# Kernel tuning notes

Hardware: AMD Instinct MI355X
Metric: run time of the kernel (lower is better)

## Reference

```python
import jax, jax.numpy as jnp
import numpy as np

IMAGE_SIZE = 1920
NMS_PRE = 3000
NMS_POST = 300
THRESHOLD = 0.5
RATIOS = (0.5, 1.0, 2.0)
SCALES = (8.0, 16.0, 32.0)


def _generate_anchors(stride, H, W):
    # Standard RPN-style grid anchors: [H, W, K, 4] in (x1, y1, x2, y2).
    ratios = jnp.asarray(RATIOS, jnp.float32)
    scales = jnp.asarray(SCALES, jnp.float32)
    ws = (stride * scales[None, :] / jnp.sqrt(ratios)[:, None]).reshape(-1)  # [K]
    hs = (stride * scales[None, :] * jnp.sqrt(ratios)[:, None]).reshape(-1)  # [K]
    cx = (jnp.arange(W, dtype=jnp.float32) + 0.5) * stride
    cy = (jnp.arange(H, dtype=jnp.float32) + 0.5) * stride
    cyg, cxg = jnp.meshgrid(cy, cx, indexing="ij")  # [H, W]
    x1 = cxg[..., None] - 0.5 * ws
    y1 = cyg[..., None] - 0.5 * hs
    x2 = cxg[..., None] + 0.5 * ws
    y2 = cyg[..., None] + 0.5 * hs
    return jnp.stack([x1, y1, x2, y2], axis=-1)  # [H, W, K, 4]


def _nms_keep(boxes, scores):
    # Greedy NMS on score-sorted boxes [P,4]; returns bool keep mask [P].
    boxes = jax.lax.stop_gradient(boxes)
    P = boxes.shape[0]
    x1, y1, x2, y2 = boxes[:, 0], boxes[:, 1], boxes[:, 2], boxes[:, 3]
    areas = (x2 - x1 + 1.0) * (y2 - y1 + 1.0)
    xx1 = jnp.maximum(x1[:, None], x1[None, :])
    yy1 = jnp.maximum(y1[:, None], y1[None, :])
    xx2 = jnp.minimum(x2[:, None], x2[None, :])
    yy2 = jnp.minimum(y2[:, None], y2[None, :])
    inter = jnp.maximum(xx2 - xx1 + 1.0, 0.0) * jnp.maximum(yy2 - yy1 + 1.0, 0.0)
    iou = inter / (areas[:, None] + areas[None, :] - inter)  # [P, P]
    idx = jnp.arange(P)

    def body(keep, i):
        sup = (iou[i] > THRESHOLD) & (idx > i) & keep[i]
        return keep & ~sup, None

    keep, _ = jax.lax.scan(body, jnp.ones((P,), bool), jnp.arange(P))
    return keep


def _select(keep, boxes, scores):
    # First NMS_POST kept entries, zero padded (matches pad_tensor).
    rank = jnp.cumsum(keep) - 1
    valid = keep & (rank < NMS_POST)
    pos = jnp.where(valid, rank, NMS_POST)  # invalid -> scratch slot
    b = jnp.zeros((NMS_POST + 1, 4), boxes.dtype).at[pos].set(
        jnp.where(valid[:, None], boxes, 0.0))[:NMS_POST]
    s = jnp.zeros((NMS_POST + 1,), scores.dtype).at[pos].set(
        jnp.where(valid, scores, 0.0))[:NMS_POST]
    return b, s


def _forward(cls_scores, bbox_deltas):
    N, K, H, W = cls_scores.shape
    stride = float(int(round(IMAGE_SIZE / float(W))))
    anchors = _generate_anchors(stride, H, W)  # [H, W, K, 4]
    # [N, 4K, H, W] -> [N, H, W, K, 4]; decode is a plain add, as in the source.
    deltas = bbox_deltas.transpose(0, 2, 3, 1).reshape(N, H, W, K, 4)
    regions = anchors[None] + deltas  # [N, H, W, K, 4]
    # permute(0,2,3,1) then permute(0,3,1,2) is the identity on cls_scores.
    scores = cls_scores.reshape(N, -1)  # [N, K*H*W]
    # Faithful replication of the torch .view memory reinterpretation:
    # contiguous [N,H,W,K,4] viewed as [N,K,4,H,W], permuted, flattened.
    regions = regions.reshape(N, K, 4, H, W).transpose(0, 3, 4, 1, 2).reshape(N, -1, 4)
    # cross_boundary(..., remove=False): clip boxes to the image.
    regions = jnp.clip(regions, 0.0, IMAGE_SIZE - 1.0)
    pre = min(NMS_PRE, scores.shape[1])
    top_scores, order = jax.lax.top_k(scores, pre)  # sorted desc, like torch.topk
    regions_top = jnp.take_along_axis(regions, order[:, :, None], axis=1)  # [N, pre, 4]
    keep = jax.vmap(_nms_keep)(regions_top, top_scores)  # [N, pre] bool
    boxes_out, scores_out = jax.vmap(_select)(keep, regions_top, top_scores)
    # Faithful to the source bug: `output[:, :, 0] = ...` inside the batch loop
    # overwrites the score column for ALL images each iteration, so the final
    # score column equals the last image's padded scores, broadcast over N.
    score_col = jnp.broadcast_to(scores_out[-1][None, :, None], (N, NMS_POST, 1))
    return jnp.concatenate([score_col, boxes_out], axis=-1)  # [N, NMS_POST, 5]


def setup_inputs() -> dict:
    key = jax.random.key(0)
    k1, k2 = jax.random.split(key)
    cls_scores = jax.random.normal(k1, (8, 9, 120, 120), dtype=jnp.float32)
    bbox_deltas = jax.random.normal(k2, (8, 36, 120, 120), dtype=jnp.float32) * 8.0
    return {"cls_scores": cls_scores, "bbox_deltas": bbox_deltas}


def reference(cls_scores, bbox_deltas):
    return _forward(cls_scores, bbox_deltas)
```

## Files before the change

### kernel.cpp

```cpp
#include <hip/hip_runtime.h>
#include <stdint.h>

#define A_TOTAL 129600
#define NBATCH 8
#define PRE 3000
#define POST 300
#define NWORD 47
#define CAP 6144
#define NTILE 1128
#define HBLK 32
#define JCHUNK 768

typedef unsigned long long u64;

__device__ __forceinline__ unsigned xform(float f) {
    unsigned b = __float_as_uint(f);
    return (b & 0x80000000u) ? ~b : (b | 0x80000000u);
}
__device__ __forceinline__ float unxform(unsigned u) {
    return __uint_as_float((u & 0x80000000u) ? (u & 0x7FFFFFFFu) : ~u);
}
__device__ __forceinline__ u64 readlane64(u64 v, int l) {
    unsigned lo = (unsigned)__builtin_amdgcn_readlane((int)(unsigned)v, l);
    unsigned hi = (unsigned)__builtin_amdgcn_readlane((int)(unsigned)(v >> 32), l);
    return ((u64)hi << 32) | lo;
}

__global__ void zero_kernel(unsigned* __restrict__ ghist, int* __restrict__ ccount,
                            int* __restrict__ grank) {
    int g = blockIdx.x * blockDim.x + threadIdx.x;
    if (g < NBATCH * 4096) ghist[g] = 0u;
    else if (g < NBATCH * 4096 + NBATCH) ccount[g - NBATCH * 4096] = 0;
    else if (g < NBATCH * 4096 + NBATCH + NBATCH * CAP)
        grank[g - NBATCH * 4096 - NBATCH] = 0;
}

__global__ __launch_bounds__(256) void hist1_kernel(const float* __restrict__ cls,
                                                    unsigned* __restrict__ ghist) {
    const int n = blockIdx.y;
    __shared__ unsigned h[4096];
    for (int i = threadIdx.x; i < 4096; i += 256) h[i] = 0u;
    __syncthreads();
    const float4* c4 = (const float4*)(cls + (size_t)n * A_TOTAL);
    const int n4 = A_TOTAL / 4;
    for (int i = blockIdx.x * 256 + threadIdx.x; i < n4; i += HBLK * 256) {
        float4 v = c4[i];
        atomicAdd(&h[xform(v.x) >> 20], 1u);
        atomicAdd(&h[xform(v.y) >> 20], 1u);
        atomicAdd(&h[xform(v.z) >> 20], 1u);
        atomicAdd(&h[xform(v.w) >> 20], 1u);
    }
    __syncthreads();
    unsigned* gh = ghist + n * 4096;
    for (int i = threadIdx.x; i < 4096; i += 256)
        if (h[i]) atomicAdd(&gh[i], h[i]);
}

__global__ __launch_bounds__(256) void pick1_kernel(const unsigned* __restrict__ ghist,
                                                    unsigned* __restrict__ state) {
    const int n = blockIdx.x;
    const int tid = threadIdx.x;
    __shared__ unsigned gsum[256];
    const unsigned* gh = ghist + n * 4096;
    unsigned s = 0;
    for (int q = 0; q < 16; ++q) s += gh[tid * 16 + q];
    gsum[tid] = s;
    __syncthreads();
    if (tid == 0) {
        unsigned acc = 0; int g = 255;
        for (; g > 0; --g) { if (acc + gsum[g] >= PRE) break; acc += gsum[g]; }
        int b = 16 * g + 15;
        for (; b >= 16 * g; --b) { if (acc + gh[b] >= PRE) break; acc += gh[b]; }
        state[n] = ((unsigned)b) << 20;
    }
}

__global__ __launch_bounds__(256) void compact_kernel(const float* __restrict__ cls,
                                                      const unsigned* __restrict__ state,
                                                      u64* __restrict__ cand,
                                                      int* __restrict__ ccount) {
    const int n = blockIdx.y;
    const int tid = threadIdx.x;
    __shared__ u64 lbuf[4096];
    __shared__ unsigned lcnt, lbase;
    if (tid == 0) lcnt = 0u;
    __syncthreads();
    const unsigned uT = state[n];
    const float4* c4 = (const float4*)(cls + (size_t)n * A_TOTAL);
    const int n4 = A_TOTAL / 4;
    for (int i = blockIdx.x * 256 + tid; i < n4; i += HBLK * 256) {
        float4 v = c4[i];
        const float* vf = (const float*)&v;
#pragma unroll
        for (int c = 0; c < 4; ++c) {
            unsigned u = xform(vf[c]);
            if (u >= uT) {
                unsigned slot = atomicAdd(&lcnt, 1u);
                if (slot < 4096u)
                    lbuf[slot] = ((u64)u << 32) | (unsigned)(~(4 * i + c));
            }
        }
    }
    __syncthreads();
    if (tid == 0) lbase = (unsigned)atomicAdd(&ccount[n], (int)min(lcnt, 4096u));
    __syncthreads();
    const unsigned cnt = min(lcnt, 4096u), base = lbase;
    u64* cd = cand + (size_t)n * CAP;
    for (unsigned j = tid; j < cnt; j += 256)
        if (base + j < CAP) cd[base + j] = lbuf[j];
}

__global__ __launch_bounds__(256) void ranksort_partial(const u64* __restrict__ cand,
                                                        const int* __restrict__ ccount,
                                                        int* __restrict__ grank) {
    const int n = blockIdx.z;
    const int C = min(ccount[n], CAP);
    if (blockIdx.x * 256 >= C) return;
    const int j0 = blockIdx.y * JCHUNK;
    if (j0 >= C) return;
    const int tid = threadIdx.x;
    __shared__ u64 k[JCHUNK];
    const u64* cd = cand + (size_t)n * CAP;
    const int jlim = min(JCHUNK, C - j0);
    for (int j = tid; j < JCHUNK; j += 256)
        k[j] = (j < jlim) ? cd[j0 + j] : 0ull;
    __syncthreads();
    const int i = blockIdx.x * 256 + tid;
    if (i >= C) return;
    const u64 key = cd[i];
    int rank = 0;
    int j = 0;
    for (; j + 8 <= JCHUNK; j += 8) {
        rank += (k[j] > key) + (k[j+1] > key) + (k[j+2] > key) + (k[j+3] > key)
              + (k[j+4] > key) + (k[j+5] > key) + (k[j+6] > key) + (k[j+7] > key);
    }
    if (rank) atomicAdd(&grank[n * CAP + i], rank);
}

__global__ __launch_bounds__(256) void rank_gather(const u64* __restrict__ cand,
                                                   const int* __restrict__ ccount,
                                                   const int* __restrict__ grank,
                                                   const float* __restrict__ bbox,
                                                   float* __restrict__ tscores,
                                                   float* __restrict__ boxes) {
    const int n = blockIdx.y;
    const int C = min(ccount[n], CAP);
    const int i = blockIdx.x * 256 + threadIdx.x;
    if (i >= C) return;
    const int rank = grank[n * CAP + i];
    if (rank >= PRE) return;
    const u64 key = cand[(size_t)n * CAP + i];
    const unsigned u = (unsigned)(key >> 32);
    const int r = (int)(~(unsigned)key);
    tscores[n * PRE + rank] = unxform(u);

    int kp = r % 9;
    int pp = r / 9;
    int s_ch = pp % 36;
    int qbase = pp / 36;
    int k2 = s_ch >> 2, j2 = s_ch & 3;
    float ratio = (k2 < 3) ? 0.5f : ((k2 < 6) ? 1.0f : 2.0f);
    int si = k2 % 3;
    float scale = (si == 0) ? 8.0f : ((si == 1) ? 16.0f : 32.0f);
    float sq = sqrtf(ratio);
    float wsk = 16.0f * scale / sq;
    float hsk = 16.0f * scale * sq;
    float* outp = boxes + ((size_t)n * PRE + rank) * 4;
#pragma unroll
    for (int j4 = 0; j4 < 4; ++j4) {
        int c = 4 * kp + j4;
        int q = c * 400 + qbase;
        int hh = q / 120, w2 = q % 120;
        float cx = (w2 + 0.5f) * 16.0f;
        float cy = (hh + 0.5f) * 16.0f;
        float a;
        if (j2 == 0)      a = cx - 0.5f * wsk;
        else if (j2 == 1) a = cy - 0.5f * hsk;
        else if (j2 == 2) a = cx + 0.5f * wsk;
        else              a = cy + 0.5f * hsk;
        float d = bbox[((size_t)n * 36 + s_ch) * 14400 + q];
        outp[j4] = fminf(fmaxf(a + d, 0.0f), 1919.0f);
    }
}

__global__ __launch_bounds__(256) void nms_mask_kernel(const float* __restrict__ boxes,
                                                       u64* __restrict__ mask) {
    const int n = blockIdx.y;
    const int t = threadIdx.x & 63;
    const int wv = threadIdx.x >> 6;
    const int T = blockIdx.x * 4 + wv;
    const bool active = (T < NTILE);
    __shared__ float cx1[4][64], cy1[4][64], cx2[4][64], cy2[4][64], car[4][64];
    int rb = 0, cb = 0;
    if (active) {
        int off = 0;
        for (int r = 0; r < NWORD; ++r) {
            int row_tiles = NWORD - r;
            if (T < off + row_tiles) { rb = r; cb = r + (T - off); break; }
            off += row_tiles;
        }
        int cj = cb * 64 + t;
        if (cj < PRE) {
            float4 b4 = *(const float4*)(boxes + ((size_t)n * PRE + cj) * 4);
            cx1[wv][t] = b4.x; cy1[wv][t] = b4.y; cx2[wv][t] = b4.z; cy2[wv][t] = b4.w;
            car[wv][t] = (b4.z - b4.x + 1.0f) * (b4.w - b4.y + 1.0f);
        }
    }
    __syncthreads();
    if (!active) return;
    int i = rb * 64 + t;
    if (i >= PRE) return;
    float4 b4 = *(const float4*)(boxes + ((size_t)n * PRE + i) * 4);
    float x1 = b4.x, y1 = b4.y, x2 = b4.z, y2 = b4.w;
    float ai = (x2 - x1 + 1.0f) * (y2 - y1 + 1.0f);
    u64 w = 0ull;
    int lim = min(64, PRE - cb * 64);
    for (int jj = 0; jj < lim; ++jj) {
        float xx1 = fmaxf(x1, cx1[wv][jj]);
        float yy1 = fmaxf(y1, cy1[wv][jj]);
        float xx2 = fminf(x2, cx2[wv][jj]);
        float yy2 = fminf(y2, cy2[wv][jj]);
        float iw = fmaxf(xx2 - xx1 + 1.0f, 0.0f);
        float ih = fmaxf(yy2 - yy1 + 1.0f, 0.0f);
        float inter = iw * ih;
        float iou = inter / (ai + car[wv][jj] - inter);
        if (iou > 0.5f) w |= (1ull << jj);
    }
    mask[((size_t)n * PRE + i) * NWORD + cb] = w;
}

#define TSTRIDE 49
__global__ __launch_bounds__(256) void nms_scan_kernel(const u64* __restrict__ mask,
                                                       const float* __restrict__ tscores,
                                                       const float* __restrict__ boxes,
                                                       float* __restrict__ out) {
    const int n = blockIdx.x;
    const int tid = threadIdx.x;
    const int lane = tid & 63;
    const int wv = tid >> 6;
    __shared__ u64 tile[2][64 * TSTRIDE];
    __shared__ int kidx[POST];
    __shared__ int s_cnt;
    const u64* mrow = mask + (size_t)n * PRE * NWORD;

    for (int idx = tid; idx < 64 * NWORD; idx += 256) {
        int r = idx / NWORD, wd = idx % NWORD;
        tile[0][r * TSTRIDE + wd] = mrow[(size_t)r * NWORD + wd];
    }
    if (tid == 0) s_cnt = 0;
    __syncthreads();

    u64 rem = 0ull;
    for (int w = 0; w < NWORD; ++w) {
        const int buf = w & 1;
        if (wv > 0 && w + 1 < NWORD) {
            const int base = 64 * (w + 1);
            for (int idx = tid - 64; idx < 64 * NWORD; idx += 192) {
                int r = idx / NWORD, wd = idx % NWORD;
                int row = base + r;
                tile[buf ^ 1][r * TSTRIDE + wd] =
                    (row < PRE) ? mrow[(size_t)row * NWORD + wd] : 0ull;
            }
        }
        if (wv == 0) {
            int cnt = s_cnt;
            const int base = 64 * w;
            const int lim = min(64, PRE - base);
            u64 vrow = (lane < lim) ? tile[buf][lane * TSTRIDE + w] : 0ull;
            u64 cur = readlane64(rem, w);
            u64 todo = ~cur;
            if (lim < 64) todo &= (1ull << lim) - 1ull;
            u64 alive = 0ull;
            while (todo) {
                int b = __ffsll((long long)todo) - 1;
                if (lane == 0) kidx[cnt] = base + b;
                alive |= 1ull << b;
                cnt++;
                if (cnt >= POST) break;
                u64 sup = readlane64(vrow, b);
                todo &= ~(sup | (1ull << b));
            }
            if (lane < NWORD) {
                u64 t2 = alive;
                while (t2) {
                    int b0 = __ffsll((long long)t2) - 1; t2 &= t2 - 1;
                    int b1 = b0, b2 = b0, b3 = b0;
                    if (t2) { b1 = __ffsll((long long)t2) - 1; t2 &= t2 - 1; }
                    if (t2) { b2 = __ffsll((long long)t2) - 1; t2 &= t2 - 1; }
                    if (t2) { b3 = __ffsll((long long)t2) - 1; t2 &= t2 - 1; }
                    u64 a0 = tile[buf][b0 * TSTRIDE + lane];
                    u64 a1 = tile[buf][b1 * TSTRIDE + lane];
                    u64 a2 = tile[buf][b2 * TSTRIDE + lane];
                    u64 a3 = tile[buf][b3 * TSTRIDE + lane];
                    rem |= (a0 | a1) | (a2 | a3);
                }
            }
            if (lane == 0) s_cnt = cnt;
        }
        __syncthreads();
        if (s_cnt >= POST) break;
    }

    const int cnt = s_cnt;
    for (int t = tid; t < POST; t += 256) {
        float* op = out + ((size_t)n * POST + t) * 5;
        if (t < cnt) {
            int i = kidx[t];
            const float* bp = boxes + ((size_t)n * PRE + i) * 4;
            op[1] = bp[0]; op[2] = bp[1]; op[3] = bp[2]; op[4] = bp[3];
        } else {
            op[1] = 0.0f; op[2] = 0.0f; op[3] = 0.0f; op[4] = 0.0f;
        }
        if (n == NBATCH - 1) {
            float sv = (t < cnt) ? tscores[n * PRE + kidx[t]] : 0.0f;
            for (int m = 0; m < NBATCH; ++m)
                out[((size_t)m * POST + t) * 5] = sv;
        }
    }
}

extern "C" void kernel_launch(void* const* d_in, const int* in_sizes, int n_in,
                              void* d_out, int out_size, void* d_ws, size_t ws_size,
                              hipStream_t stream) {
    const float* cls = (const float*)d_in[0];
    const float* bbox = (const float*)d_in[1];
    float* out = (float*)d_out;

    char* p = (char*)d_ws;
    u64* mask = (u64*)p;
    unsigned* ghist = (unsigned*)p;
    unsigned* state = (unsigned*)(p + 131072);
    int* ccount = (int*)(p + 131200);
    u64* cand = (u64*)(p + 131584);
    int* grank = (int*)(p + 524800);
    float* tscores = (float*)(p + 9024000);
    float* boxes = (float*)(p + 9120000);
    (void)ws_size; (void)n_in; (void)in_sizes; (void)out_size;

    zero_kernel<<<(NBATCH * 4096 + NBATCH + NBATCH * CAP + 255) / 256, 256, 0, stream>>>(ghist, ccount, grank);
    hist1_kernel<<<dim3(HBLK, NBATCH), 256, 0, stream>>>(cls, ghist);
    pick1_kernel<<<NBATCH, 256, 0, stream>>>(ghist, state);
    compact_kernel<<<dim3(HBLK, NBATCH), 256, 0, stream>>>(cls, state, cand, ccount);
    ranksort_partial<<<dim3(CAP / 256, CAP / JCHUNK, NBATCH), 256, 0, stream>>>(cand, ccount, grank);
    rank_gather<<<dim3(CAP / 256, NBATCH), 256, 0, stream>>>(cand, ccount, grank, bbox, tscores, boxes);
    nms_mask_kernel<<<dim3((NTILE + 3) / 4, NBATCH), 256, 0, stream>>>(boxes, mask);
    nms_scan_kernel<<<NBATCH, 256, 0, stream>>>(mask, tscores, boxes, out);
}
```

Before: 182.3 us.

## Widen NMS scan windows to 192 rows and replace rank atomics with partial sums

The NMS scan now processes 192-row windows, three 64-bit words at a time, so the block runs 16 barrier-separated iterations instead of 47. The tile is stored unpadded and copied with float4 loads. The rank atomics are replaced by per-chunk partial rank arrays that rank_gather sums, which removes the zeroing kernel in favour of a memset plus resetting ccount in pick1. The trade-off is much larger LDS use (about 144 KB) and more register pressure in the serial scan loop.

```diff
diff --git a/kernel.cpp b/kernel.cpp
--- a/kernel.cpp
+++ b/kernel.cpp
@@ -10,6 +10,9 @@
 #define NTILE 1128
 #define HBLK 32
 #define JCHUNK 768
+#define NJC 8
+#define WW 192
+#define NWIN 16
 
 typedef unsigned long long u64;
 
@@ -24,15 +27,6 @@
     unsigned lo = (unsigned)__builtin_amdgcn_readlane((int)(unsigned)v, l);
     unsigned hi = (unsigned)__builtin_amdgcn_readlane((int)(unsigned)(v >> 32), l);
     return ((u64)hi << 32) | lo;
-}
-
-__global__ void zero_kernel(unsigned* __restrict__ ghist, int* __restrict__ ccount,
-                            int* __restrict__ grank) {
-    int g = blockIdx.x * blockDim.x + threadIdx.x;
-    if (g < NBATCH * 4096) ghist[g] = 0u;
-    else if (g < NBATCH * 4096 + NBATCH) ccount[g - NBATCH * 4096] = 0;
-    else if (g < NBATCH * 4096 + NBATCH + NBATCH * CAP)
-        grank[g - NBATCH * 4096 - NBATCH] = 0;
 }
 
 __global__ __launch_bounds__(256) void hist1_kernel(const float* __restrict__ cls,
@@ -57,7 +51,8 @@
 }
 
 __global__ __launch_bounds__(256) void pick1_kernel(const unsigned* __restrict__ ghist,
-                                                    unsigned* __restrict__ state) {
+                                                    unsigned* __restrict__ state,
+                                                    int* __restrict__ ccount) {
     const int n = blockIdx.x;
     const int tid = threadIdx.x;
     __shared__ unsigned gsum[256];
@@ -72,6 +67,7 @@
         int b = 16 * g + 15;
         for (; b >= 16 * g; --b) { if (acc + gh[b] >= PRE) break; acc += gh[b]; }
         state[n] = ((unsigned)b) << 20;
+        ccount[n] = 0;
     }
 }
 
@@ -112,7 +108,7 @@
 
 __global__ __launch_bounds__(256) void ranksort_partial(const u64* __restrict__ cand,
                                                         const int* __restrict__ ccount,
-                                                        int* __restrict__ grank) {
+                                                        int* __restrict__ grank_part) {
     const int n = blockIdx.z;
     const int C = min(ccount[n], CAP);
     if (blockIdx.x * 256 >= C) return;
@@ -134,12 +130,12 @@
         rank += (k[j] > key) + (k[j+1] > key) + (k[j+2] > key) + (k[j+3] > key)
               + (k[j+4] > key) + (k[j+5] > key) + (k[j+6] > key) + (k[j+7] > key);
     }
-    if (rank) atomicAdd(&grank[n * CAP + i], rank);
+    grank_part[((size_t)n * NJC + blockIdx.y) * CAP + i] = rank;
 }
 
 __global__ __launch_bounds__(256) void rank_gather(const u64* __restrict__ cand,
                                                    const int* __restrict__ ccount,
-                                                   const int* __restrict__ grank,
+                                                   const int* __restrict__ grank_part,
                                                    const float* __restrict__ bbox,
                                                    float* __restrict__ tscores,
                                                    float* __restrict__ boxes) {
@@ -147,7 +143,10 @@
     const int C = min(ccount[n], CAP);
     const int i = blockIdx.x * 256 + threadIdx.x;
     if (i >= C) return;
-    const int rank = grank[n * CAP + i];
+    const int nj = (C + JCHUNK - 1) / JCHUNK;
+    int rank = 0;
+    for (int jc = 0; jc < nj; ++jc)
+        rank += grank_part[((size_t)n * NJC + jc) * CAP + i];
     if (rank >= PRE) return;
     const u64 key = cand[(size_t)n * CAP + i];
     const unsigned u = (unsigned)(key >> 32);
@@ -229,7 +228,6 @@
     mask[((size_t)n * PRE + i) * NWORD + cb] = w;
 }
 
-#define TSTRIDE 49
 __global__ __launch_bounds__(256) void nms_scan_kernel(const u64* __restrict__ mask,
                                                        const float* __restrict__ tscores,
                                                        const float* __restrict__ boxes,
@@ -238,61 +236,89 @@
     const int tid = threadIdx.x;
     const int lane = tid & 63;
     const int wv = tid >> 6;
-    __shared__ u64 tile[2][64 * TSTRIDE];
+    __shared__ u64 tile[2][WW * NWORD];
     __shared__ int kidx[POST];
     __shared__ int s_cnt;
     const u64* mrow = mask + (size_t)n * PRE * NWORD;
 
-    for (int idx = tid; idx < 64 * NWORD; idx += 256) {
-        int r = idx / NWORD, wd = idx % NWORD;
-        tile[0][r * TSTRIDE + wd] = mrow[(size_t)r * NWORD + wd];
+    {
+        const float4* src = (const float4*)mrow;
+        float4* dst = (float4*)tile[0];
+        for (int i = tid; i < WW * NWORD / 2; i += 256) dst[i] = src[i];
     }
     if (tid == 0) s_cnt = 0;
     __syncthreads();
 
     u64 rem = 0ull;
-    for (int w = 0; w < NWORD; ++w) {
+    for (int w = 0; w < NWIN; ++w) {
         const int buf = w & 1;
-        if (wv > 0 && w + 1 < NWORD) {
-            const int base = 64 * (w + 1);
-            for (int idx = tid - 64; idx < 64 * NWORD; idx += 192) {
-                int r = idx / NWORD, wd = idx % NWORD;
-                int row = base + r;
-                tile[buf ^ 1][r * TSTRIDE + wd] =
-                    (row < PRE) ? mrow[(size_t)row * NWORD + wd] : 0ull;
-            }
+        const int base = WW * w;
+        if (wv > 0 && w + 1 < NWIN) {
+            const int nbase = base + WW;
+            const int nrows = min(WW, PRE - nbase);
+            const float4* src = (const float4*)(mrow + (size_t)nbase * NWORD);
+            float4* dst = (float4*)tile[buf ^ 1];
+            const int n4 = nrows * NWORD / 2;
+            for (int i = tid - 64; i < n4; i += 192) dst[i] = src[i];
         }
         if (wv == 0) {
             int cnt = s_cnt;
-            const int base = 64 * w;
-            const int lim = min(64, PRE - base);
-            u64 vrow = (lane < lim) ? tile[buf][lane * TSTRIDE + w] : 0ull;
-            u64 cur = readlane64(rem, w);
-            u64 todo = ~cur;
-            if (lim < 64) todo &= (1ull << lim) - 1ull;
-            u64 alive = 0ull;
-            while (todo) {
-                int b = __ffsll((long long)todo) - 1;
-                if (lane == 0) kidx[cnt] = base + b;
-                alive |= 1ull << b;
+            const int lim = min(WW, PRE - base);
+            const int w0 = 3 * w;
+            const bool q2ok = (w0 + 2 < NWORD);
+            u64 v00, v01, v02, v10, v11, v12, v20, v21, v22;
+            {
+                const u64* t0 = &tile[buf][(size_t)lane * NWORD + w0];
+                const u64* t1 = &tile[buf][(size_t)(lane + 64) * NWORD + w0];
+                const u64* t2 = &tile[buf][(size_t)(lane + 128) * NWORD + w0];
+                v00 = t0[0]; v01 = t0[1]; v02 = q2ok ? t0[2] : 0ull;
+                v10 = t1[0]; v11 = t1[1]; v12 = q2ok ? t1[2] : 0ull;
+                v20 = t2[0]; v21 = t2[1]; v22 = q2ok ? t2[2] : 0ull;
+            }
+            u64 todo0 = ~readlane64(rem, w0);
+            u64 todo1 = ~readlane64(rem, w0 + 1);
+            u64 todo2 = q2ok ? ~readlane64(rem, w0 + 2) : 0ull;
+            if (lim < 64)       { todo0 &= (1ull << lim) - 1; todo1 = 0; todo2 = 0; }
+            else if (lim < 128) { todo1 &= (1ull << (lim - 64)) - 1; todo2 = 0; }
+            else if (lim < 192) { todo2 &= (1ull << (lim - 128)) - 1; }
+            u64 alive0 = 0, alive1 = 0, alive2 = 0;
+            while (todo0 | todo1 | todo2) {
+                int q, b;
+                if (todo0)      { q = 0; b = __ffsll((long long)todo0) - 1; }
+                else if (todo1) { q = 1; b = __ffsll((long long)todo1) - 1; }
+                else            { q = 2; b = __ffsll((long long)todo2) - 1; }
+                const int p = q * 64 + b;
+                if (lane == 0) kidx[cnt] = base + p;
+                if (q == 0) alive0 |= 1ull << b;
+                else if (q == 1) alive1 |= 1ull << b;
+                else alive2 |= 1ull << b;
                 cnt++;
                 if (cnt >= POST) break;
-                u64 sup = readlane64(vrow, b);
-                todo &= ~(sup | (1ull << b));
+                u64 s0, s1, s2;
+                if (q == 0)      { s0 = readlane64(v00, b); s1 = readlane64(v01, b); s2 = readlane64(v02, b); }
+                else if (q == 1) { s0 = readlane64(v10, b); s1 = readlane64(v11, b); s2 = readlane64(v12, b); }
+                else             { s0 = readlane64(v20, b); s1 = readlane64(v21, b); s2 = readlane64(v22, b); }
+                todo0 &= ~s0; todo1 &= ~s1; todo2 &= ~s2;
+                if (q == 0) todo0 &= ~(1ull << b);
+                else if (q == 1) todo1 &= ~(1ull << b);
+                else todo2 &= ~(1ull << b);
             }
             if (lane < NWORD) {
-                u64 t2 = alive;
-                while (t2) {
-                    int b0 = __ffsll((long long)t2) - 1; t2 &= t2 - 1;
-                    int b1 = b0, b2 = b0, b3 = b0;
-                    if (t2) { b1 = __ffsll((long long)t2) - 1; t2 &= t2 - 1; }
-                    if (t2) { b2 = __ffsll((long long)t2) - 1; t2 &= t2 - 1; }
-                    if (t2) { b3 = __ffsll((long long)t2) - 1; t2 &= t2 - 1; }
-                    u64 a0 = tile[buf][b0 * TSTRIDE + lane];
-                    u64 a1 = tile[buf][b1 * TSTRIDE + lane];
-                    u64 a2 = tile[buf][b2 * TSTRIDE + lane];
-                    u64 a3 = tile[buf][b3 * TSTRIDE + lane];
-                    rem |= (a0 | a1) | (a2 | a3);
+                for (int q = 0; q < 3; ++q) {
+                    u64 t2m = (q == 0) ? alive0 : (q == 1) ? alive1 : alive2;
+                    const int roff = q * 64;
+                    while (t2m) {
+                        int b0 = __ffsll((long long)t2m) - 1; t2m &= t2m - 1;
+                        int b1 = b0, b2 = b0, b3 = b0;
+                        if (t2m) { b1 = __ffsll((long long)t2m) - 1; t2m &= t2m - 1; }
+                        if (t2m) { b2 = __ffsll((long long)t2m) - 1; t2m &= t2m - 1; }
+                        if (t2m) { b3 = __ffsll((long long)t2m) - 1; t2m &= t2m - 1; }
+                        u64 a0 = tile[buf][(size_t)(roff + b0) * NWORD + lane];
+                        u64 a1 = tile[buf][(size_t)(roff + b1) * NWORD + lane];
+                        u64 a2 = tile[buf][(size_t)(roff + b2) * NWORD + lane];
+                        u64 a3 = tile[buf][(size_t)(roff + b3) * NWORD + lane];
+                        rem |= (a0 | a1) | (a2 | a3);
+                    }
                 }
             }
             if (lane == 0) s_cnt = cnt;
@@ -332,17 +358,17 @@
     unsigned* state = (unsigned*)(p + 131072);
     int* ccount = (int*)(p + 131200);
     u64* cand = (u64*)(p + 131584);
-    int* grank = (int*)(p + 524800);
+    int* grank_part = (int*)(p + 524800);
     float* tscores = (float*)(p + 9024000);
     float* boxes = (float*)(p + 9120000);
     (void)ws_size; (void)n_in; (void)in_sizes; (void)out_size;
 
-    zero_kernel<<<(NBATCH * 4096 + NBATCH + NBATCH * CAP + 255) / 256, 256, 0, stream>>>(ghist, ccount, grank);
+    hipMemsetAsync(ghist, 0, 131072, stream);
     hist1_kernel<<<dim3(HBLK, NBATCH), 256, 0, stream>>>(cls, ghist);
-    pick1_kernel<<<NBATCH, 256, 0, stream>>>(ghist, state);
+    pick1_kernel<<<NBATCH, 256, 0, stream>>>(ghist, state, ccount);
     compact_kernel<<<dim3(HBLK, NBATCH), 256, 0, stream>>>(cls, state, cand, ccount);
-    ranksort_partial<<<dim3(CAP / 256, CAP / JCHUNK, NBATCH), 256, 0, stream>>>(cand, ccount, grank);
-    rank_gather<<<dim3(CAP / 256, NBATCH), 256, 0, stream>>>(cand, ccount, grank, bbox, tscores, boxes);
+    ranksort_partial<<<dim3(CAP / 256, NJC, NBATCH), 256, 0, stream>>>(cand, ccount, grank_part);
+    rank_gather<<<dim3(CAP / 256, NBATCH), 256, 0, stream>>>(cand, ccount, grank_part, bbox, tscores, boxes);
     nms_mask_kernel<<<dim3((NTILE + 3) / 4, NBATCH), 256, 0, stream>>>(boxes, mask);
     nms_scan_kernel<<<NBATCH, 256, 0, stream>>>(mask, tscores, boxes, out);
 }
```

Measured after the change: 225.5 us. 1.24x slower.

## Fuse RPN proposal pipeline into one cooperative persistent kernel with grid syncs

Applied to the files above, without the earlier changes.

Replaces eight separate kernel launches with a single cooperative kernel of 256 blocks that runs histogram, threshold pick, compaction, rank sort, gather, NMS mask and scan phases separated by grid.sync. Global atomics on the histogram and rank arrays are replaced with per-slice and per-chunk partial arrays that are reduced in later phases, which also removes the zeroing kernel. The aim is to remove launch gaps and atomic traffic. In exchange it adds grid-wide barriers, and the later phases run on a fixed 256-block grid whose work is looped over.

```diff
diff --git a/kernel.cpp b/kernel.cpp
--- a/kernel.cpp
+++ b/kernel.cpp
@@ -1,5 +1,8 @@
 #include <hip/hip_runtime.h>
+#include <hip/hip_cooperative_groups.h>
 #include <stdint.h>
+
+namespace cg = cooperative_groups;
 
 #define A_TOTAL 129600
 #define NBATCH 8
@@ -8,8 +11,11 @@
 #define NWORD 47
 #define CAP 6144
 #define NTILE 1128
-#define HBLK 32
+#define NSLICE 32
 #define JCHUNK 768
+#define NJC 8
+#define TSTRIDE 49
+#define SMEM_U64 (2 * 64 * TSTRIDE)
 
 typedef unsigned long long u64;
 
@@ -26,295 +32,304 @@
     return ((u64)hi << 32) | lo;
 }
 
-__global__ void zero_kernel(unsigned* __restrict__ ghist, int* __restrict__ ccount,
-                            int* __restrict__ grank) {
-    int g = blockIdx.x * blockDim.x + threadIdx.x;
-    if (g < NBATCH * 4096) ghist[g] = 0u;
-    else if (g < NBATCH * 4096 + NBATCH) ccount[g - NBATCH * 4096] = 0;
-    else if (g < NBATCH * 4096 + NBATCH + NBATCH * CAP)
-        grank[g - NBATCH * 4096 - NBATCH] = 0;
-}
-
-__global__ __launch_bounds__(256) void hist1_kernel(const float* __restrict__ cls,
-                                                    unsigned* __restrict__ ghist) {
-    const int n = blockIdx.y;
-    __shared__ unsigned h[4096];
-    for (int i = threadIdx.x; i < 4096; i += 256) h[i] = 0u;
-    __syncthreads();
-    const float4* c4 = (const float4*)(cls + (size_t)n * A_TOTAL);
-    const int n4 = A_TOTAL / 4;
-    for (int i = blockIdx.x * 256 + threadIdx.x; i < n4; i += HBLK * 256) {
-        float4 v = c4[i];
-        atomicAdd(&h[xform(v.x) >> 20], 1u);
-        atomicAdd(&h[xform(v.y) >> 20], 1u);
-        atomicAdd(&h[xform(v.z) >> 20], 1u);
-        atomicAdd(&h[xform(v.w) >> 20], 1u);
-    }
-    __syncthreads();
-    unsigned* gh = ghist + n * 4096;
-    for (int i = threadIdx.x; i < 4096; i += 256)
-        if (h[i]) atomicAdd(&gh[i], h[i]);
-}
-
-__global__ __launch_bounds__(256) void pick1_kernel(const unsigned* __restrict__ ghist,
-                                                    unsigned* __restrict__ state) {
-    const int n = blockIdx.x;
+__global__ __launch_bounds__(256) void mega_kernel(
+    const float* __restrict__ cls, const float* __restrict__ bbox,
+    unsigned* __restrict__ ghist_part, unsigned* __restrict__ state,
+    int* __restrict__ ccount, u64* __restrict__ cand,
+    int* __restrict__ grank_part, float* __restrict__ tscores,
+    float* __restrict__ boxes, u64* __restrict__ mask,
+    float* __restrict__ out)
+{
+    cg::grid_group grid = cg::this_grid();
+    const int blk = blockIdx.x;
     const int tid = threadIdx.x;
-    __shared__ unsigned gsum[256];
-    const unsigned* gh = ghist + n * 4096;
-    unsigned s = 0;
-    for (int q = 0; q < 16; ++q) s += gh[tid * 16 + q];
-    gsum[tid] = s;
-    __syncthreads();
-    if (tid == 0) {
-        unsigned acc = 0; int g = 255;
-        for (; g > 0; --g) { if (acc + gsum[g] >= PRE) break; acc += gsum[g]; }
-        int b = 16 * g + 15;
-        for (; b >= 16 * g; --b) { if (acc + gh[b] >= PRE) break; acc += gh[b]; }
-        state[n] = ((unsigned)b) << 20;
-    }
-}
-
-__global__ __launch_bounds__(256) void compact_kernel(const float* __restrict__ cls,
-                                                      const unsigned* __restrict__ state,
-                                                      u64* __restrict__ cand,
-                                                      int* __restrict__ ccount) {
-    const int n = blockIdx.y;
-    const int tid = threadIdx.x;
-    __shared__ u64 lbuf[4096];
-    __shared__ unsigned lcnt, lbase;
-    if (tid == 0) lcnt = 0u;
-    __syncthreads();
-    const unsigned uT = state[n];
-    const float4* c4 = (const float4*)(cls + (size_t)n * A_TOTAL);
-    const int n4 = A_TOTAL / 4;
-    for (int i = blockIdx.x * 256 + tid; i < n4; i += HBLK * 256) {
-        float4 v = c4[i];
-        const float* vf = (const float*)&v;
+
+    __shared__ u64 smem[SMEM_U64];
+    __shared__ int kidx[POST];
+    __shared__ unsigned s_misc[4];
+
+    {
+        const int n = blk & 7, slice = blk >> 3;
+        unsigned* h = (unsigned*)smem;
+        for (int i = tid; i < 4096; i += 256) h[i] = 0u;
+        __syncthreads();
+        const float4* c4 = (const float4*)(cls + (size_t)n * A_TOTAL);
+        const int n4 = A_TOTAL / 4;
+        for (int i = slice * 256 + tid; i < n4; i += NSLICE * 256) {
+            float4 v = c4[i];
+            atomicAdd(&h[xform(v.x) >> 20], 1u);
+            atomicAdd(&h[xform(v.y) >> 20], 1u);
+            atomicAdd(&h[xform(v.z) >> 20], 1u);
+            atomicAdd(&h[xform(v.w) >> 20], 1u);
+        }
+        __syncthreads();
+        unsigned* gh = ghist_part + ((size_t)(n * NSLICE + slice)) * 4096;
+        for (int i = tid; i < 4096; i += 256) gh[i] = h[i];
+    }
+    grid.sync();
+    if (blk < NBATCH) {
+        unsigned* h = (unsigned*)smem;
+        unsigned* gsum = h + 4096;
+        const unsigned* gh = ghist_part + (size_t)blk * NSLICE * 4096;
+        for (int bin = tid; bin < 4096; bin += 256) {
+            unsigned s = 0;
+            for (int sl = 0; sl < NSLICE; ++sl) s += gh[sl * 4096 + bin];
+            h[bin] = s;
+        }
+        __syncthreads();
+        {
+            unsigned s = 0;
+            for (int q = 0; q < 16; ++q) s += h[tid * 16 + q];
+            gsum[tid] = s;
+        }
+        __syncthreads();
+        if (tid == 0) {
+            unsigned acc = 0; int g = 255;
+            for (; g > 0; --g) { if (acc + gsum[g] >= PRE) break; acc += gsum[g]; }
+            int b = 16 * g + 15;
+            for (; b >= 16 * g; --b) { if (acc + h[b] >= PRE) break; acc += h[b]; }
+            state[blk] = ((unsigned)b) << 20;
+            ccount[blk] = 0;
+        }
+    }
+    grid.sync();
+    {
+        const int n = blk & 7, slice = blk >> 3;
+        u64* lbuf = smem;
+        if (tid == 0) s_misc[0] = 0u;
+        __syncthreads();
+        const unsigned uT = state[n];
+        const float4* c4 = (const float4*)(cls + (size_t)n * A_TOTAL);
+        const int n4 = A_TOTAL / 4;
+        for (int i = slice * 256 + tid; i < n4; i += NSLICE * 256) {
+            float4 v = c4[i];
+            const float* vf = (const float*)&v;
 #pragma unroll
-        for (int c = 0; c < 4; ++c) {
-            unsigned u = xform(vf[c]);
-            if (u >= uT) {
-                unsigned slot = atomicAdd(&lcnt, 1u);
-                if (slot < 4096u)
-                    lbuf[slot] = ((u64)u << 32) | (unsigned)(~(4 * i + c));
-            }
-        }
-    }
-    __syncthreads();
-    if (tid == 0) lbase = (unsigned)atomicAdd(&ccount[n], (int)min(lcnt, 4096u));
-    __syncthreads();
-    const unsigned cnt = min(lcnt, 4096u), base = lbase;
-    u64* cd = cand + (size_t)n * CAP;
-    for (unsigned j = tid; j < cnt; j += 256)
-        if (base + j < CAP) cd[base + j] = lbuf[j];
-}
-
-__global__ __launch_bounds__(256) void ranksort_partial(const u64* __restrict__ cand,
-                                                        const int* __restrict__ ccount,
-                                                        int* __restrict__ grank) {
-    const int n = blockIdx.z;
-    const int C = min(ccount[n], CAP);
-    if (blockIdx.x * 256 >= C) return;
-    const int j0 = blockIdx.y * JCHUNK;
-    if (j0 >= C) return;
-    const int tid = threadIdx.x;
-    __shared__ u64 k[JCHUNK];
-    const u64* cd = cand + (size_t)n * CAP;
-    const int jlim = min(JCHUNK, C - j0);
-    for (int j = tid; j < JCHUNK; j += 256)
-        k[j] = (j < jlim) ? cd[j0 + j] : 0ull;
-    __syncthreads();
-    const int i = blockIdx.x * 256 + tid;
-    if (i >= C) return;
-    const u64 key = cd[i];
-    int rank = 0;
-    int j = 0;
-    for (; j + 8 <= JCHUNK; j += 8) {
-        rank += (k[j] > key) + (k[j+1] > key) + (k[j+2] > key) + (k[j+3] > key)
-              + (k[j+4] > key) + (k[j+5] > key) + (k[j+6] > key) + (k[j+7] > key);
-    }
-    if (rank) atomicAdd(&grank[n * CAP + i], rank);
-}
-
-__global__ __launch_bounds__(256) void rank_gather(const u64* __restrict__ cand,
-                                                   const int* __restrict__ ccount,
-                                                   const int* __restrict__ grank,
-                                                   const float* __restrict__ bbox,
-                                                   float* __restrict__ tscores,
-                                                   float* __restrict__ boxes) {
-    const int n = blockIdx.y;
-    const int C = min(ccount[n], CAP);
-    const int i = blockIdx.x * 256 + threadIdx.x;
-    if (i >= C) return;
-    const int rank = grank[n * CAP + i];
-    if (rank >= PRE) return;
-    const u64 key = cand[(size_t)n * CAP + i];
-    const unsigned u = (unsigned)(key >> 32);
-    const int r = (int)(~(unsigned)key);
-    tscores[n * PRE + rank] = unxform(u);
-
-    int kp = r % 9;
-    int pp = r / 9;
-    int s_ch = pp % 36;
-    int qbase = pp / 36;
-    int k2 = s_ch >> 2, j2 = s_ch & 3;
-    float ratio = (k2 < 3) ? 0.5f : ((k2 < 6) ? 1.0f : 2.0f);
-    int si = k2 % 3;
-    float scale = (si == 0) ? 8.0f : ((si == 1) ? 16.0f : 32.0f);
-    float sq = sqrtf(ratio);
-    float wsk = 16.0f * scale / sq;
-    float hsk = 16.0f * scale * sq;
-    float* outp = boxes + ((size_t)n * PRE + rank) * 4;
+            for (int c = 0; c < 4; ++c) {
+                unsigned u = xform(vf[c]);
+                if (u >= uT) {
+                    unsigned slot = atomicAdd(&s_misc[0], 1u);
+                    if (slot < 4096u)
+                        lbuf[slot] = ((u64)u << 32) | (unsigned)(~(4 * i + c));
+                }
+            }
+        }
+        __syncthreads();
+        if (tid == 0)
+            s_misc[1] = (unsigned)atomicAdd(&ccount[n], (int)min(s_misc[0], 4096u));
+        __syncthreads();
+        const unsigned cnt = min(s_misc[0], 4096u), base = s_misc[1];
+        u64* cd = cand + (size_t)n * CAP;
+        for (unsigned j = tid; j < cnt; j += 256)
+            if (base + j < CAP) cd[base + j] = lbuf[j];
+        __syncthreads();
+    }
+    grid.sync();
+    for (int k = 0; k < 6; ++k) {
+        const int unit = blk + 256 * k;
+        const int n = unit / 192;
+        const int rest = unit % 192;
+        const int jc = rest / 24;
+        const int iblk = rest % 24;
+        const int C = min(ccount[n], CAP);
+        const int j0 = jc * JCHUNK;
+        u64* kk = smem;
+        const u64* cd = cand + (size_t)n * CAP;
+        const int jlim = min(JCHUNK, C - j0);
+        for (int j = tid; j < JCHUNK; j += 256)
+            kk[j] = (j < jlim) ? cd[j0 + j] : 0ull;
+        __syncthreads();
+        const int i = iblk * 256 + tid;
+        if (i < C && j0 < C) {
+            const u64 key = cd[i];
+            int rank = 0;
+            for (int j = 0; j + 8 <= JCHUNK; j += 8) {
+                rank += (kk[j] > key) + (kk[j+1] > key) + (kk[j+2] > key) + (kk[j+3] > key)
+                      + (kk[j+4] > key) + (kk[j+5] > key) + (kk[j+6] > key) + (kk[j+7] > key);
+            }
+            grank_part[((size_t)n * NJC + jc) * CAP + i] = rank;
+        }
+        __syncthreads();
+    }
+    grid.sync();
+    if (blk < 192) {
+        const int n = blk / 24;
+        const int i = (blk % 24) * 256 + tid;
+        const int C = min(ccount[n], CAP);
+        if (i < C) {
+            const int nj = (C + JCHUNK - 1) / JCHUNK;
+            int rank = 0;
+            for (int jc = 0; jc < nj; ++jc)
+                rank += grank_part[((size_t)n * NJC + jc) * CAP + i];
+            if (rank < PRE) {
+                const u64 key = cand[(size_t)n * CAP + i];
+                const unsigned u = (unsigned)(key >> 32);
+                const int r = (int)(~(unsigned)key);
+                tscores[n * PRE + rank] = unxform(u);
+                int kp = r % 9;
+                int pp = r / 9;
+                int s_ch = pp % 36;
+                int qbase = pp / 36;
+                int k2 = s_ch >> 2, j2 = s_ch & 3;
+                float ratio = (k2 < 3) ? 0.5f : ((k2 < 6) ? 1.0f : 2.0f);
+                int si = k2 % 3;
+                float scale = (si == 0) ? 8.0f : ((si == 1) ? 16.0f : 32.0f);
+                float sq = sqrtf(ratio);
+                float wsk = 16.0f * scale / sq;
+                float hsk = 16.0f * scale * sq;
+                float* outp = boxes + ((size_t)n * PRE + rank) * 4;
 #pragma unroll
-    for (int j4 = 0; j4 < 4; ++j4) {
-        int c = 4 * kp + j4;
-        int q = c * 400 + qbase;
-        int hh = q / 120, w2 = q % 120;
-        float cx = (w2 + 0.5f) * 16.0f;
-        float cy = (hh + 0.5f) * 16.0f;
-        float a;
-        if (j2 == 0)      a = cx - 0.5f * wsk;
-        else if (j2 == 1) a = cy - 0.5f * hsk;
-        else if (j2 == 2) a = cx + 0.5f * wsk;
-        else              a = cy + 0.5f * hsk;
-        float d = bbox[((size_t)n * 36 + s_ch) * 14400 + q];
-        outp[j4] = fminf(fmaxf(a + d, 0.0f), 1919.0f);
-    }
-}
-
-__global__ __launch_bounds__(256) void nms_mask_kernel(const float* __restrict__ boxes,
-                                                       u64* __restrict__ mask) {
-    const int n = blockIdx.y;
-    const int t = threadIdx.x & 63;
-    const int wv = threadIdx.x >> 6;
-    const int T = blockIdx.x * 4 + wv;
-    const bool active = (T < NTILE);
-    __shared__ float cx1[4][64], cy1[4][64], cx2[4][64], cy2[4][64], car[4][64];
-    int rb = 0, cb = 0;
-    if (active) {
-        int off = 0;
-        for (int r = 0; r < NWORD; ++r) {
-            int row_tiles = NWORD - r;
-            if (T < off + row_tiles) { rb = r; cb = r + (T - off); break; }
-            off += row_tiles;
-        }
-        int cj = cb * 64 + t;
-        if (cj < PRE) {
-            float4 b4 = *(const float4*)(boxes + ((size_t)n * PRE + cj) * 4);
-            cx1[wv][t] = b4.x; cy1[wv][t] = b4.y; cx2[wv][t] = b4.z; cy2[wv][t] = b4.w;
-            car[wv][t] = (b4.z - b4.x + 1.0f) * (b4.w - b4.y + 1.0f);
-        }
-    }
-    __syncthreads();
-    if (!active) return;
-    int i = rb * 64 + t;
-    if (i >= PRE) return;
-    float4 b4 = *(const float4*)(boxes + ((size_t)n * PRE + i) * 4);
-    float x1 = b4.x, y1 = b4.y, x2 = b4.z, y2 = b4.w;
-    float ai = (x2 - x1 + 1.0f) * (y2 - y1 + 1.0f);
-    u64 w = 0ull;
-    int lim = min(64, PRE - cb * 64);
-    for (int jj = 0; jj < lim; ++jj) {
-        float xx1 = fmaxf(x1, cx1[wv][jj]);
-        float yy1 = fmaxf(y1, cy1[wv][jj]);
-        float xx2 = fminf(x2, cx2[wv][jj]);
-        float yy2 = fminf(y2, cy2[wv][jj]);
-        float iw = fmaxf(xx2 - xx1 + 1.0f, 0.0f);
-        float ih = fmaxf(yy2 - yy1 + 1.0f, 0.0f);
-        float inter = iw * ih;
-        float iou = inter / (ai + car[wv][jj] - inter);
-        if (iou > 0.5f) w |= (1ull << jj);
-    }
-    mask[((size_t)n * PRE + i) * NWORD + cb] = w;
-}
-
-#define TSTRIDE 49
-__global__ __launch_bounds__(256) void nms_scan_kernel(const u64* __restrict__ mask,
-                                                       const float* __restrict__ tscores,
-                                                       const float* __restrict__ boxes,
-                                                       float* __restrict__ out) {
-    const int n = blockIdx.x;
-    const int tid = threadIdx.x;
-    const int lane = tid & 63;
-    const int wv = tid >> 6;
-    __shared__ u64 tile[2][64 * TSTRIDE];
-    __shared__ int kidx[POST];
-    __shared__ int s_cnt;
-    const u64* mrow = mask + (size_t)n * PRE * NWORD;
-
-    for (int idx = tid; idx < 64 * NWORD; idx += 256) {
-        int r = idx / NWORD, wd = idx % NWORD;
-        tile[0][r * TSTRIDE + wd] = mrow[(size_t)r * NWORD + wd];
-    }
-    if (tid == 0) s_cnt = 0;
-    __syncthreads();
-
-    u64 rem = 0ull;
-    for (int w = 0; w < NWORD; ++w) {
-        const int buf = w & 1;
-        if (wv > 0 && w + 1 < NWORD) {
-            const int base = 64 * (w + 1);
-            for (int idx = tid - 64; idx < 64 * NWORD; idx += 192) {
-                int r = idx / NWORD, wd = idx % NWORD;
-                int row = base + r;
-                tile[buf ^ 1][r * TSTRIDE + wd] =
-                    (row < PRE) ? mrow[(size_t)row * NWORD + wd] : 0ull;
-            }
-        }
-        if (wv == 0) {
-            int cnt = s_cnt;
-            const int base = 64 * w;
-            const int lim = min(64, PRE - base);
-            u64 vrow = (lane < lim) ? tile[buf][lane * TSTRIDE + w] : 0ull;
-            u64 cur = readlane64(rem, w);
-            u64 todo = ~cur;
-            if (lim < 64) todo &= (1ull << lim) - 1ull;
-            u64 alive = 0ull;
-            while (todo) {
-                int b = __ffsll((long long)todo) - 1;
-                if (lane == 0) kidx[cnt] = base + b;
-                alive |= 1ull << b;
-                cnt++;
-                if (cnt >= POST) break;
-                u64 sup = readlane64(vrow, b);
-                todo &= ~(sup | (1ull << b));
-            }
-            if (lane < NWORD) {
-                u64 t2 = alive;
-                while (t2) {
-                    int b0 = __ffsll((long long)t2) - 1; t2 &= t2 - 1;
-                    int b1 = b0, b2 = b0, b3 = b0;
-                    if (t2) { b1 = __ffsll((long long)t2) - 1; t2 &= t2 - 1; }
-                    if (t2) { b2 = __ffsll((long long)t2) - 1; t2 &= t2 - 1; }
-                    if (t2) { b3 = __ffsll((long long)t2) - 1; t2 &= t2 - 1; }
-                    u64 a0 = tile[buf][b0 * TSTRIDE + lane];
-                    u64 a1 = tile[buf][b1 * TSTRIDE + lane];
-                    u64 a2 = tile[buf][b2 * TSTRIDE + lane];
-                    u64 a3 = tile[buf][b3 * TSTRIDE + lane];
-                    rem |= (a0 | a1) | (a2 | a3);
-                }
-            }
-            if (lane == 0) s_cnt = cnt;
-        }
-        __syncthreads();
-        if (s_cnt >= POST) break;
-    }
-
-    const int cnt = s_cnt;
-    for (int t = tid; t < POST; t += 256) {
-        float* op = out + ((size_t)n * POST + t) * 5;
-        if (t < cnt) {
-            int i = kidx[t];
-            const float* bp = boxes + ((size_t)n * PRE + i) * 4;
-            op[1] = bp[0]; op[2] = bp[1]; op[3] = bp[2]; op[4] = bp[3];
-        } else {
-            op[1] = 0.0f; op[2] = 0.0f; op[3] = 0.0f; op[4] = 0.0f;
-        }
-        if (n == NBATCH - 1) {
-            float sv = (t < cnt) ? tscores[n * PRE + kidx[t]] : 0.0f;
-            for (int m = 0; m < NBATCH; ++m)
-                out[((size_t)m * POST + t) * 5] = sv;
+                for (int j4 = 0; j4 < 4; ++j4) {
+                    int c = 4 * kp + j4;
+                    int q = c * 400 + qbase;
+                    int hh = q / 120, w2 = q % 120;
+                    float cx = (w2 + 0.5f) * 16.0f;
+                    float cy = (hh + 0.5f) * 16.0f;
+                    float a;
+                    if (j2 == 0)      a = cx - 0.5f * wsk;
+                    else if (j2 == 1) a = cy - 0.5f * hsk;
+                    else if (j2 == 2) a = cx + 0.5f * wsk;
+                    else              a = cy + 0.5f * hsk;
+                    float d = bbox[((size_t)n * 36 + s_ch) * 14400 + q];
+                    outp[j4] = fminf(fmaxf(a + d, 0.0f), 1919.0f);
+                }
+            }
+        }
+    }
+    grid.sync();
+    for (int k = 0; k < 9; ++k) {
+        const int unit = blk + 256 * k;
+        const int t = tid & 63;
+        const int wv = tid >> 6;
+        float* fs = (float*)smem;
+        float* cx1 = fs, *cy1 = fs + 256, *cx2 = fs + 512, *cy2 = fs + 768, *car = fs + 1024;
+        const int n = unit / 282;
+        const int xu = unit % 282;
+        const int T = xu * 4 + wv;
+        const bool active = (unit < 2256) && (T < NTILE);
+        int rb = 0, cb = 0;
+        if (active) {
+            int off = 0;
+            for (int r = 0; r < NWORD; ++r) {
+                int row_tiles = NWORD - r;
+                if (T < off + row_tiles) { rb = r; cb = r + (T - off); break; }
+                off += row_tiles;
+            }
+            int cj = cb * 64 + t;
+            if (cj < PRE) {
+                float4 b4 = *(const float4*)(boxes + ((size_t)n * PRE + cj) * 4);
+                cx1[wv * 64 + t] = b4.x; cy1[wv * 64 + t] = b4.y;
+                cx2[wv * 64 + t] = b4.z; cy2[wv * 64 + t] = b4.w;
+                car[wv * 64 + t] = (b4.z - b4.x + 1.0f) * (b4.w - b4.y + 1.0f);
+            }
+        }
+        __syncthreads();
+        if (active) {
+            int i = rb * 64 + t;
+            if (i < PRE) {
+                float4 b4 = *(const float4*)(boxes + ((size_t)n * PRE + i) * 4);
+                float x1 = b4.x, y1 = b4.y, x2 = b4.z, y2 = b4.w;
+                float ai = (x2 - x1 + 1.0f) * (y2 - y1 + 1.0f);
+                u64 w = 0ull;
+                int lim = min(64, PRE - cb * 64);
+                for (int jj = 0; jj < lim; ++jj) {
+                    float xx1 = fmaxf(x1, cx1[wv * 64 + jj]);
+                    float yy1 = fmaxf(y1, cy1[wv * 64 + jj]);
+                    float xx2 = fminf(x2, cx2[wv * 64 + jj]);
+                    float yy2 = fminf(y2, cy2[wv * 64 + jj]);
+                    float iw = fmaxf(xx2 - xx1 + 1.0f, 0.0f);
+                    float ih = fmaxf(yy2 - yy1 + 1.0f, 0.0f);
+                    float inter = iw * ih;
+                    float iou = inter / (ai + car[wv * 64 + jj] - inter);
+                    if (iou > 0.5f) w |= (1ull << jj);
+                }
+                mask[((size_t)n * PRE + i) * NWORD + cb] = w;
+            }
+        }
+        __syncthreads();
+    }
+    grid.sync();
+    if (blk >= NBATCH) return;
+    {
+        const int n = blk;
+        const int lane = tid & 63;
+        const int wv = tid >> 6;
+        u64 (*tile)[64 * TSTRIDE] = (u64(*)[64 * TSTRIDE])smem;
+        const u64* mrow = mask + (size_t)n * PRE * NWORD;
+
+        for (int idx = tid; idx < 64 * NWORD; idx += 256) {
+            int r = idx / NWORD, wd = idx % NWORD;
+            tile[0][r * TSTRIDE + wd] = mrow[(size_t)r * NWORD + wd];
+        }
+        if (tid == 0) s_misc[0] = 0u;
+        __syncthreads();
+
+        u64 rem = 0ull;
+        for (int w = 0; w < NWORD; ++w) {
+            const int buf = w & 1;
+            if (wv > 0 && w + 1 < NWORD) {
+                const int base = 64 * (w + 1);
+                for (int idx = tid - 64; idx < 64 * NWORD; idx += 192) {
+                    int r = idx / NWORD, wd = idx % NWORD;
+                    int row = base + r;
+                    tile[buf ^ 1][r * TSTRIDE + wd] =
+                        (row < PRE) ? mrow[(size_t)row * NWORD + wd] : 0ull;
+                }
+            }
+            if (wv == 0) {
+                int cnt = (int)s_misc[0];
+                const int base = 64 * w;
+                const int lim = min(64, PRE - base);
+                u64 vrow = (lane < lim) ? tile[buf][lane * TSTRIDE + w] : 0ull;
+                u64 cur = readlane64(rem, w);
+                u64 todo = ~cur;
+                if (lim < 64) todo &= (1ull << lim) - 1ull;
+                u64 alive = 0ull;
+                while (todo) {
+                    int b = __ffsll((long long)todo) - 1;
+                    if (lane == 0) kidx[cnt] = base + b;
+                    alive |= 1ull << b;
+                    cnt++;
+                    if (cnt >= POST) break;
+                    u64 sup = readlane64(vrow, b);
+                    todo &= ~(sup | (1ull << b));
+                }
+                if (lane < NWORD) {
+                    u64 t2 = alive;
+                    while (t2) {
+                        int b0 = __ffsll((long long)t2) - 1; t2 &= t2 - 1;
+                        int b1 = b0, b2 = b0, b3 = b0;
+                        if (t2) { b1 = __ffsll((long long)t2) - 1; t2 &= t2 - 1; }
+                        if (t2) { b2 = __ffsll((long long)t2) - 1; t2 &= t2 - 1; }
+                        if (t2) { b3 = __ffsll((long long)t2) - 1; t2 &= t2 - 1; }
+                        u64 a0 = tile[buf][b0 * TSTRIDE + lane];
+                        u64 a1 = tile[buf][b1 * TSTRIDE + lane];
+                        u64 a2 = tile[buf][b2 * TSTRIDE + lane];
+                        u64 a3 = tile[buf][b3 * TSTRIDE + lane];
+                        rem |= (a0 | a1) | (a2 | a3);
+                    }
+                }
+                if (lane == 0) s_misc[0] = (unsigned)cnt;
+            }
+            __syncthreads();
+            if ((int)s_misc[0] >= POST) break;
+        }
+
+        const int cnt = (int)s_misc[0];
+        for (int t = tid; t < POST; t += 256) {
+            float* op = out + ((size_t)n * POST + t) * 5;
+            if (t < cnt) {
+                int i = kidx[t];
+                const float* bp = boxes + ((size_t)n * PRE + i) * 4;
+                op[1] = bp[0]; op[2] = bp[1]; op[3] = bp[2]; op[4] = bp[3];
+            } else {
+                op[1] = 0.0f; op[2] = 0.0f; op[3] = 0.0f; op[4] = 0.0f;
+            }
+            if (n == NBATCH - 1) {
+                float sv = (t < cnt) ? tscores[n * PRE + kidx[t]] : 0.0f;
+                for (int m = 0; m < NBATCH; ++m)
+                    out[((size_t)m * POST + t) * 5] = sv;
+            }
         }
     }
 }
@@ -328,21 +343,17 @@
 
     char* p = (char*)d_ws;
     u64* mask = (u64*)p;
-    unsigned* ghist = (unsigned*)p;
-    unsigned* state = (unsigned*)(p + 131072);
-    int* ccount = (int*)(p + 131200);
-    u64* cand = (u64*)(p + 131584);
-    int* grank = (int*)(p + 524800);
+    unsigned* ghist_part = (unsigned*)p;
+    unsigned* state = (unsigned*)(p + 4194304);
+    int* ccount = (int*)(p + 4194336);
+    u64* cand = (u64*)(p + 4194368);
+    int* grank_part = (int*)(p + 4587584);
     float* tscores = (float*)(p + 9024000);
     float* boxes = (float*)(p + 9120000);
     (void)ws_size; (void)n_in; (void)in_sizes; (void)out_size;
 
-    zero_kernel<<<(NBATCH * 4096 + NBATCH + NBATCH * CAP + 255) / 256, 256, 0, stream>>>(ghist, ccount, grank);
-    hist1_kernel<<<dim3(HBLK, NBATCH), 256, 0, stream>>>(cls, ghist);
-    pick1_kernel<<<NBATCH, 256, 0, stream>>>(ghist, state);
-    compact_kernel<<<dim3(HBLK, NBATCH), 256, 0, stream>>>(cls, state, cand, ccount);
-    ranksort_partial<<<dim3(CAP / 256, CAP / JCHUNK, NBATCH), 256, 0, stream>>>(cand, ccount, grank);
-    rank_gather<<<dim3(CAP / 256, NBATCH), 256, 0, stream>>>(cand, ccount, grank, bbox, tscores, boxes);
-    nms_mask_kernel<<<dim3((NTILE + 3) / 4, NBATCH), 256, 0, stream>>>(boxes, mask);
-    nms_scan_kernel<<<NBATCH, 256, 0, stream>>>(mask, tscores, boxes, out);
-}
+    void* args[] = { (void*)&cls, (void*)&bbox, (void*)&ghist_part, (void*)&state,
+                     (void*)&ccount, (void*)&cand, (void*)&grank_part,
+                     (void*)&tscores, (void*)&boxes, (void*)&mask, (void*)&out };
+    hipLaunchCooperativeKernel((void*)mega_kernel, dim3(256), dim3(256), args, 0, stream);
+}
```

Measured after the change: 414.2 us. 127% more time.
